# Optimization experiments

Measured on AMD Instinct MI355X. Metric: run time of the kernel, lower is better.

Reference implementation:

```python
import jax, jax.numpy as jnp
import numpy as np
from jax import lax

B, H, W, C = 16, 256, 256, 1
LOC_C = 31            # channels out of localization network
BN_EPS = 1e-3         # Keras BatchNormalization default epsilon
NEG_SLOPE = 0.1       # LeakyReLU slope


def _conv_relu(x, k, b):
    y = lax.conv_general_dilated(x, k, (1, 1), 'SAME',
                                 dimension_numbers=('NHWC', 'HWIO', 'NHWC'))
    return jax.nn.relu(y + b)


def _maxpool2(x):
    return lax.reduce_window(x, -jnp.inf, lax.max, (1, 2, 2, 1), (1, 2, 2, 1), 'VALID')


def _resize_nearest(x, out_h, out_w):
    # tf.image.resize(..., method='nearest') with half-pixel centers
    b, h, w, c = x.shape
    ih = jnp.floor((jnp.arange(out_h) + 0.5) * h / out_h).astype(jnp.int32)
    iw = jnp.floor((jnp.arange(out_w) + 0.5) * w / out_w).astype(jnp.int32)
    return x[:, ih][:, :, iw]


def _generate_grid(theta, height, width):
    # base grid in [-1, 1], x varies along width, y along height
    xs = jnp.arange(width, dtype=jnp.float32) / (width - 1) * 2.0 - 1.0
    ys = jnp.arange(height, dtype=jnp.float32) / (height - 1) * 2.0 - 1.0
    gx, gy = jnp.meshgrid(xs, ys)                      # (H, W)
    grid = jnp.stack([gx, gy], axis=-1).reshape(height * width, 2)  # (HW, 2)
    th = theta.reshape(-1, 2, 3)
    A = th[:, :, :2]                                   # (B, 2, 2)
    t = th[:, :, 2]                                    # (B, 2)
    # NOTE: source does grid @ A (not A @ grid) -- replicate exactly
    tg = jnp.einsum('nc,bcd->bnd', grid, A) + t[:, None, :]
    return tg.reshape(-1, height, width, 2)


def _sampler(img, grid):
    b, h, w, c = img.shape
    x = 0.5 * ((grid[..., 0] + 1.0) * (w - 1))
    y = 0.5 * ((grid[..., 1] + 1.0) * (h - 1))
    x0 = jnp.floor(x); x1 = x0 + 1.0
    y0 = jnp.floor(y); y1 = y0 + 1.0
    x0 = jnp.clip(x0, 0.0, w - 1.0); x1 = jnp.clip(x1, 0.0, w - 1.0)
    y0 = jnp.clip(y0, 0.0, h - 1.0); y1 = jnp.clip(y1, 0.0, h - 1.0)
    wa = (x1 - x) * (y1 - y)
    wb = (x1 - x) * (y - y0)
    wc = (x - x0) * (y1 - y)
    wd = (x - x0) * (y - y0)
    xi0 = x0.astype(jnp.int32); xi1 = x1.astype(jnp.int32)
    yi0 = y0.astype(jnp.int32); yi1 = y1.astype(jnp.int32)
    img_flat = img.reshape(b, h * w, c)

    def gather(yi, xi):
        idx = (yi * w + xi).reshape(b, h * w, 1)       # (B, HW, 1)
        return jnp.take_along_axis(img_flat, idx, axis=1).reshape(b, h, w, c)

    Ia = gather(yi0, xi0)
    Ib = gather(yi1, xi0)
    Ic = gather(yi0, xi1)
    Id = gather(yi1, xi1)
    return (wa[..., None] * Ia + wb[..., None] * Ib
            + wc[..., None] * Ic + wd[..., None] * Id)


def setup_inputs() -> dict:
    key = jax.random.key(0)
    ks = jax.random.split(key, 16)
    s = 0.05
    feat = (H // 8) * (W // 8) * LOC_C  # 31744 flattened localization features
    return {
        'x': jax.random.normal(ks[0], (B, H, W, C), jnp.float32),
        'conv1_k': jax.random.normal(ks[1], (3, 3, C, 8), jnp.float32) * s,
        'conv1_b': jnp.zeros((8,), jnp.float32),
        'conv2_k': jax.random.normal(ks[2], (3, 3, 8, 16), jnp.float32) * s,
        'conv2_b': jnp.zeros((16,), jnp.float32),
        'conv3_k': jax.random.normal(ks[3], (3, 3, 16, LOC_C), jnp.float32) * s,
        'conv3_b': jnp.zeros((LOC_C,), jnp.float32),
        'bn_gamma': 1.0 + 0.1 * jax.random.normal(ks[4], (feat,), jnp.float32),
        'bn_beta': 0.1 * jax.random.normal(ks[5], (feat,), jnp.float32),
        'bn_mean': jnp.zeros((feat,), jnp.float32),
        'bn_var': jnp.ones((feat,), jnp.float32),
        'd1_k': jax.random.normal(ks[6], (feat, 64), jnp.float32) * 0.01,
        'd1_b': jnp.zeros((64,), jnp.float32),
        'd2_k': jax.random.normal(ks[7], (64, 96), jnp.float32) * s,
        'd2_b': jnp.zeros((96,), jnp.float32),
        'd3_k': jax.random.normal(ks[8], (96, 6), jnp.float32) * 0.01,
        'd3_b': jnp.array([1, 0, 0, 0, 1, 0], jnp.float32),
    }


def reference(x, conv1_k, conv1_b, conv2_k, conv2_b, conv3_k, conv3_b,
              bn_gamma, bn_beta, bn_mean, bn_var,
              d1_k, d1_b, d2_k, d2_b, d3_k, d3_b):
    # localization network: (conv-relu, pool) x3 -> (B, H/8, W/8, 31)
    xi = _maxpool2(_conv_relu(x, conv1_k, conv1_b))
    xi = _maxpool2(_conv_relu(xi, conv2_k, conv2_b))
    x_intermediate = _maxpool2(_conv_relu(xi, conv3_k, conv3_b))
    # transformation parameter network (BN in inference mode, dropout = identity)
    f = x_intermediate.reshape(x.shape[0], -1)
    f = (f - bn_mean) * jax.lax.rsqrt(bn_var + BN_EPS) * bn_gamma + bn_beta
    f = jax.nn.relu(f @ d1_k + d1_b)
    f = jax.nn.relu(f @ d2_k + d2_b)
    theta = f @ d3_k + d3_b                            # (B, 6)
    grid = _generate_grid(theta, H, W)                 # (B, H, W, 2)
    loc_up = _resize_nearest(x_intermediate, H, W)     # (B, H, W, 31)
    xc = jnp.concatenate([x, loc_up], axis=-1)         # (B, H, W, 32)
    out = _sampler(xc, grid)
    return jnp.where(out >= 0, out, NEG_SLOPE * out)
```

## Files before the change

kernel.cpp:

```cpp
#include <hip/hip_runtime.h>


#define NEG_SLOPE 0.1f
#define BN_EPS 1e-3f

typedef float vfloat4 __attribute__((ext_vector_type(4)));

__device__ __forceinline__ void fma8(float pv, const float* __restrict__ wk,
                                     float* __restrict__ acc) {
#pragma unroll
    for (int co = 0; co < 8; ++co) acc[co] = fmaf(pv, wk[co], acc[co]);
}

__global__ __launch_bounds__(256, 4) void st_conv1(const float* __restrict__ x,
                                                   const float* __restrict__ w,
                                                   const float* __restrict__ bias,
                                                   float* __restrict__ outA) {
    int idx = blockIdx.x * 256 + threadIdx.x;
    int px = idx & 127, py = (idx >> 7) & 127, b = idx >> 14;
    const float* xb = x + b * 65536;
    int iy0 = 2 * py - 1, ix0 = 2 * px - 1;
    float p[16];
#pragma unroll
    for (int r = 0; r < 4; ++r) {
        int iy = iy0 + r;
        bool oky = (iy >= 0) && (iy < 256);
#pragma unroll
        for (int cc = 0; cc < 4; ++cc) {
            int ix = ix0 + cc;
            bool ok = oky && (ix >= 0) && (ix < 256);
            p[r * 4 + cc] = ok ? xb[iy * 256 + ix] : 0.0f;
        }
    }
    float m[8];
#pragma unroll
    for (int co = 0; co < 8; ++co) m[co] = -1e30f;
#pragma unroll
    for (int oy = 0; oy < 2; ++oy)
#pragma unroll
        for (int ox = 0; ox < 2; ++ox) {
            float acc[8];
#pragma unroll
            for (int co = 0; co < 8; ++co) acc[co] = 0.0f;
#pragma unroll
            for (int ky = 0; ky < 3; ++ky)
#pragma unroll
                for (int kx = 0; kx < 3; ++kx)
                    fma8(p[(oy + ky) * 4 + (ox + kx)], w + (ky * 3 + kx) * 8, acc);
#pragma unroll
            for (int co = 0; co < 8; ++co) m[co] = fmaxf(m[co], acc[co]);
        }
    float4 o0, o1;
    float r0 = m[0] + bias[0], r1 = m[1] + bias[1], r2 = m[2] + bias[2], r3 = m[3] + bias[3];
    float r4 = m[4] + bias[4], r5 = m[5] + bias[5], r6 = m[6] + bias[6], r7 = m[7] + bias[7];
    o0.x = r0 > 0.f ? r0 : 0.f; o0.y = r1 > 0.f ? r1 : 0.f;
    o0.z = r2 > 0.f ? r2 : 0.f; o0.w = r3 > 0.f ? r3 : 0.f;
    o1.x = r4 > 0.f ? r4 : 0.f; o1.y = r5 > 0.f ? r5 : 0.f;
    o1.z = r6 > 0.f ? r6 : 0.f; o1.w = r7 > 0.f ? r7 : 0.f;
    *(float4*)(outA + idx * 8) = o0;
    *(float4*)(outA + idx * 8 + 4) = o1;
}

__global__ __launch_bounds__(256, 2) void st_conv2(const float* __restrict__ A,
                                                   const float* __restrict__ w,
                                                   const float* __restrict__ bias,
                                                   float* __restrict__ outB) {
    int t = threadIdx.x;
    int lane = t & 63;
    int half = __builtin_amdgcn_readfirstlane((t >> 6) & 1);
    int pixel = blockIdx.x * 128 + ((t >> 7) << 6) + lane;
    int px = pixel & 63, py = (pixel >> 6) & 63, b = pixel >> 12;
    const float* Ab = A + b * 128 * 128 * 8;
    int iy0 = 2 * py - 1, ix0 = 2 * px - 1;
    int cobase = half * 8;
    float acc[4][8];
#pragma unroll
    for (int pos = 0; pos < 4; ++pos)
#pragma unroll
        for (int co = 0; co < 8; ++co) acc[pos][co] = 0.0f;

    const float4 z4 = {0.f, 0.f, 0.f, 0.f};
#pragma unroll
    for (int ciq = 0; ciq < 2; ++ciq) {
        float4 p[16];
#pragma unroll
        for (int r = 0; r < 4; ++r) {
            int iy = iy0 + r;
            bool oky = (iy >= 0) && (iy < 128);
#pragma unroll
            for (int cc = 0; cc < 4; ++cc) {
                int ix = ix0 + cc;
                bool ok = oky && (ix >= 0) && (ix < 128);
                p[r * 4 + cc] = ok ? *(const float4*)(Ab + ((iy * 128 + ix) * 8 + ciq * 4))
                                   : z4;
            }
        }
#pragma unroll
        for (int oy = 0; oy < 2; ++oy)
#pragma unroll
            for (int ox = 0; ox < 2; ++ox)
#pragma unroll
                for (int ky = 0; ky < 3; ++ky)
#pragma unroll
                    for (int kx = 0; kx < 3; ++kx) {
                        float4 pv = p[(oy + ky) * 4 + (ox + kx)];
                        const float* wk = w + ((ky * 3 + kx) * 8 + ciq * 4) * 16 + cobase;
                        float* a = acc[oy * 2 + ox];
                        fma8(pv.x, wk, a);
                        fma8(pv.y, wk + 16, a);
                        fma8(pv.z, wk + 32, a);
                        fma8(pv.w, wk + 48, a);
                    }
    }
    float* o = outB + pixel * 16 + cobase;
#pragma unroll
    for (int co = 0; co < 8; ++co) {
        float m = fmaxf(fmaxf(acc[0][co], acc[1][co]),
                        fmaxf(acc[2][co], acc[3][co]));
        m += bias[cobase + co];
        o[co] = m > 0.0f ? m : 0.0f;
    }
}

__global__ __launch_bounds__(256, 4) void st_conv3(const float* __restrict__ Bf,
                                                   const float* __restrict__ w,
                                                   const float* __restrict__ bias,
                                                   float* __restrict__ outC) {
    int t = threadIdx.x;
    int lane = t & 63;
    int q = __builtin_amdgcn_readfirstlane(t >> 6);
    int cobase = q * 8;
    if (cobase > 23) cobase = 23;
    int pixel = blockIdx.x * 64 + lane;
    int ix = pixel & 63, iy = (pixel >> 6) & 63, b = pixel >> 12;
    const float* Bb = Bf + b * 64 * 64 * 16;
    float acc[8];
#pragma unroll
    for (int co = 0; co < 8; ++co) acc[co] = 0.0f;

    const float4 z4 = {0.f, 0.f, 0.f, 0.f};
#pragma unroll
    for (int ciq = 0; ciq < 4; ++ciq) {
        float4 p[9];
#pragma unroll
        for (int ky = 0; ky < 3; ++ky) {
            int y = iy + ky - 1;
            bool oky = (y >= 0) && (y < 64);
#pragma unroll
            for (int kx = 0; kx < 3; ++kx) {
                int xx = ix + kx - 1;
                bool ok = oky && (xx >= 0) && (xx < 64);
                p[ky * 3 + kx] = ok ? *(const float4*)(Bb + ((y * 64 + xx) * 16 + ciq * 4))
                                    : z4;
            }
        }
#pragma unroll
        for (int k = 0; k < 9; ++k) {
            float4 pv = p[k];
            const float* wk = w + (k * 16 + ciq * 4) * 31 + cobase;
            fma8(pv.x, wk, acc);
            fma8(pv.y, wk + 31, acc);
            fma8(pv.z, wk + 62, acc);
            fma8(pv.w, wk + 93, acc);
        }
    }
    float* o = outC + pixel * 32 + cobase;
#pragma unroll
    for (int co = 0; co < 8; ++co) {
        float v = acc[co] + bias[cobase + co];
        o[co] = v > 0.0f ? v : 0.0f;
    }
}

__global__ __launch_bounds__(256) void st_pool3(const float* __restrict__ C3p,
                                                const float* __restrict__ gamma,
                                                const float* __restrict__ beta,
                                                const float* __restrict__ mean,
                                                const float* __restrict__ var,
                                                float* __restrict__ xip,
                                                float* __restrict__ fprime) {
    int idx = blockIdx.x * 256 + threadIdx.x;
    int quad = idx & 7;
    int pp = idx >> 3;
    int b = pp >> 10;
    int cell = pp & 1023;
    int py = cell >> 5, px = cell & 31;
    const float* Cb = C3p + (b * 4096) * 32 + quad * 4;
    float4 v00 = *(const float4*)(Cb + ((2 * py) * 64 + 2 * px) * 32);
    float4 v01 = *(const float4*)(Cb + ((2 * py) * 64 + 2 * px + 1) * 32);
    float4 v10 = *(const float4*)(Cb + ((2 * py + 1) * 64 + 2 * px) * 32);
    float4 v11 = *(const float4*)(Cb + ((2 * py + 1) * 64 + 2 * px + 1) * 32);
    float4 m;
    m.x = fmaxf(fmaxf(v00.x, v01.x), fmaxf(v10.x, v11.x));
    m.y = fmaxf(fmaxf(v00.y, v01.y), fmaxf(v10.y, v11.y));
    m.z = fmaxf(fmaxf(v00.z, v01.z), fmaxf(v10.z, v11.z));
    m.w = fmaxf(fmaxf(v00.w, v01.w), fmaxf(v10.w, v11.w));
    *(float4*)(xip + (b * 1024 + cell) * 32 + quad * 4) = m;
    int c0 = quad * 4;
    float mv[4] = {m.x, m.y, m.z, m.w};
#pragma unroll
    for (int c = 0; c < 4; ++c) {
        int co = c0 + c;
        if (co < 31) {
            int j = cell * 31 + co;
            float sc = gamma[j] * rsqrtf(var[j] + BN_EPS);
            fprime[b * 31744 + j] = (mv[c] - mean[j]) * sc + beta[j];
        }
    }
}

__global__ __launch_bounds__(256) void st_d1(const float* __restrict__ fp,
                                             const float* __restrict__ k1,
                                             float* __restrict__ partial) {
    int t = threadIdx.x, s = blockIdx.x;
    int o = t & 63;
    int sub = t >> 6;
    int subu = __builtin_amdgcn_readfirstlane(sub);
    int j0 = s * 124 + subu * 31;
    float acc[16];
#pragma unroll
    for (int b = 0; b < 16; ++b) acc[b] = 0.0f;
#pragma unroll 4
    for (int jj = 0; jj < 31; ++jj) {
        int j = j0 + jj;
        float kv = k1[j * 64 + o];
        const float* fpj = fp + j;
#pragma unroll
        for (int b = 0; b < 16; ++b)
            acc[b] = fmaf(fpj[b * 31744], kv, acc[b]);
    }
    __shared__ float red[4][16][64];
#pragma unroll
    for (int b = 0; b < 16; ++b) red[sub][b][o] = acc[b];
    __syncthreads();
    if (sub == 0) {
#pragma unroll
        for (int b = 0; b < 16; ++b) {
            float v = red[0][b][o] + red[1][b][o] + red[2][b][o] + red[3][b][o];
            partial[(s * 64 + o) * 16 + b] = v;
        }
    }
}

__global__ __launch_bounds__(256) void st_d1b(const float* __restrict__ partial,
                                              const float* __restrict__ bias,
                                              float* __restrict__ h1) {
    int gid = blockIdx.x * 256 + threadIdx.x;
    int o = gid >> 4, b = gid & 15;
    float s = 0.0f;
#pragma unroll 8
    for (int sl = 0; sl < 256; ++sl) s += partial[(sl * 64 + o) * 16 + b];
    s += bias[o];
    h1[b * 64 + o] = s > 0.0f ? s : 0.0f;
}

__global__ __launch_bounds__(128) void st_theta(const float* __restrict__ h1,
                                                const float* __restrict__ k2,
                                                const float* __restrict__ b2,
                                                const float* __restrict__ k3,
                                                const float* __restrict__ b3,
                                                float* __restrict__ theta) {
    int b = blockIdx.x, t = threadIdx.x;
    __shared__ float h2[96];
    if (t < 96) {
        float s = b2[t];
        for (int i = 0; i < 64; ++i) s = fmaf(h1[b * 64 + i], k2[i * 96 + t], s);
        h2[t] = s > 0.0f ? s : 0.0f;
    }
    __syncthreads();
    if (t < 6) {
        float s = b3[t];
        for (int i = 0; i < 96; ++i) s = fmaf(h2[i], k3[i * 6 + t], s);
        theta[b * 6 + t] = s;
    }
}

__global__ __launch_bounds__(256, 4) void st_sample(const float* __restrict__ x,
                                                    const float* __restrict__ xip,
                                                    const float* __restrict__ theta,
                                                    float* __restrict__ out) {
    __shared__ float smem[256 * 34];
    int t = threadIdx.x;
    int p = blockIdx.x * 256 + t;
    int ow = p & 255, oh = (p >> 8) & 255;
    int b = blockIdx.x >> 8;

    const float* th = theta + b * 6;
    float t0 = th[0], t1 = th[1], t2 = th[2], t3 = th[3], t4 = th[4], t5 = th[5];
    float gx = (float)ow * (2.0f / 255.0f) - 1.0f;
    float gy = (float)oh * (2.0f / 255.0f) - 1.0f;
    float sx = gx * t0 + gy * t3 + t2;
    float sy = gx * t1 + gy * t4 + t5;
    float xf = 0.5f * ((sx + 1.0f) * 255.0f);
    float yf = 0.5f * ((sy + 1.0f) * 255.0f);
    float x0 = floorf(xf), y0 = floorf(yf);
    float x1 = x0 + 1.0f, y1 = y0 + 1.0f;
    x0 = fminf(fmaxf(x0, 0.0f), 255.0f);
    x1 = fminf(fmaxf(x1, 0.0f), 255.0f);
    y0 = fminf(fmaxf(y0, 0.0f), 255.0f);
    y1 = fminf(fmaxf(y1, 0.0f), 255.0f);
    float wa = (x1 - xf) * (y1 - yf);
    float wb = (x1 - xf) * (yf - y0);
    float wc = (xf - x0) * (y1 - yf);
    float wd = (xf - x0) * (yf - y0);
    int xi0 = (int)x0, xi1 = (int)x1, yi0 = (int)y0, yi1 = (int)y1;

    const float* xb = x + b * 65536;
    float Ia = xb[yi0 * 256 + xi0];
    float Ib = xb[yi1 * 256 + xi0];
    float Ic = xb[yi0 * 256 + xi1];
    float Id = xb[yi1 * 256 + xi1];
    float fine = wa * Ia + wb * Ib + wc * Ic + wd * Id;
    fine = fine >= 0.0f ? fine : NEG_SLOPE * fine;

    const float* cellbase = xip + (b << 15);
    const float4* pa = (const float4*)(cellbase + (((yi0 >> 3) << 5) + (xi0 >> 3)) * 32);
    const float4* pb = (const float4*)(cellbase + (((yi1 >> 3) << 5) + (xi0 >> 3)) * 32);
    const float4* pc = (const float4*)(cellbase + (((yi0 >> 3) << 5) + (xi1 >> 3)) * 32);
    const float4* pd = (const float4*)(cellbase + (((yi1 >> 3) << 5) + (xi1 >> 3)) * 32);

    int sbase = t * 34;
    smem[sbase] = fine;
#pragma unroll
    for (int k = 0; k < 8; ++k) {
        float4 va = pa[k], vb = pb[k], vc = pc[k], vd = pd[k];
        float vx = fmaf(wa, va.x, fmaf(wb, vb.x, fmaf(wc, vc.x, wd * vd.x)));
        float vy = fmaf(wa, va.y, fmaf(wb, vb.y, fmaf(wc, vc.y, wd * vd.y)));
        float vz = fmaf(wa, va.z, fmaf(wb, vb.z, fmaf(wc, vc.z, wd * vd.z)));
        float vw = fmaf(wa, va.w, fmaf(wb, vb.w, fmaf(wc, vc.w, wd * vd.w)));
        vx = vx >= 0.0f ? vx : NEG_SLOPE * vx;
        vy = vy >= 0.0f ? vy : NEG_SLOPE * vy;
        vz = vz >= 0.0f ? vz : NEG_SLOPE * vz;
        vw = vw >= 0.0f ? vw : NEG_SLOPE * vw;
        smem[sbase + 1 + 4 * k]     = vx;
        smem[sbase + 2 + 4 * k]     = vy;
        smem[sbase + 3 + 4 * k]     = vz;
        smem[sbase + 4 + 4 * k]     = vw;
    }
    __syncthreads();

    vfloat4* ob = (vfloat4*)(out + blockIdx.x * 8192);
#pragma unroll
    for (int i = 0; i < 8; ++i) {
        int g = i * 256 + t;
        int row = g >> 3, col = 4 * (g & 7);
        float2 lo = *(const float2*)&smem[row * 34 + col];
        float2 hi = *(const float2*)&smem[row * 34 + col + 2];
        vfloat4 v = {lo.x, lo.y, hi.x, hi.y};
        __builtin_nontemporal_store(v, ob + g);
    }
}

extern "C" void kernel_launch(void* const* d_in, const int* in_sizes, int n_in,
                              void* d_out, int out_size, void* d_ws, size_t ws_size,
                              hipStream_t stream) {
    const float* x     = (const float*)d_in[0];
    const float* c1k   = (const float*)d_in[1];
    const float* c1b   = (const float*)d_in[2];
    const float* c2k   = (const float*)d_in[3];
    const float* c2b   = (const float*)d_in[4];
    const float* c3k   = (const float*)d_in[5];
    const float* c3b   = (const float*)d_in[6];
    const float* gamma = (const float*)d_in[7];
    const float* beta  = (const float*)d_in[8];
    const float* mean  = (const float*)d_in[9];
    const float* var   = (const float*)d_in[10];
    const float* d1k   = (const float*)d_in[11];
    const float* d1b   = (const float*)d_in[12];
    const float* d2k   = (const float*)d_in[13];
    const float* d2b   = (const float*)d_in[14];
    const float* d3k   = (const float*)d_in[15];
    const float* d3b   = (const float*)d_in[16];
    float* out = (float*)d_out;
    float* ws  = (float*)d_ws;

    float* A       = ws;
    float* Bf      = ws + 2097152;
    float* C3p     = ws;
    float* xip     = ws + 2097152;
    float* fprime  = ws + 3145728;
    float* partial = ws + 3653632;
    float* h1      = ws + 3915776;
    float* theta   = ws + 3916800;

    st_conv1<<<1024, 256, 0, stream>>>(x, c1k, c1b, A);
    st_conv2<<<512, 256, 0, stream>>>(A, c2k, c2b, Bf);
    st_conv3<<<1024, 256, 0, stream>>>(Bf, c3k, c3b, C3p);
    st_pool3<<<512, 256, 0, stream>>>(C3p, gamma, beta, mean, var, xip, fprime);
    st_d1<<<256, 256, 0, stream>>>(fprime, d1k, partial);
    st_d1b<<<4, 256, 0, stream>>>(partial, d1b, h1);
    st_theta<<<16, 128, 0, stream>>>(h1, d2k, d2b, d3k, d3b, theta);
    st_sample<<<4096, 256, 0, stream>>>(x, xip, theta, out);
}
```

Measured before the change: 279.4 us.

## Fuse conv3 with maxpool and BN, split sampler channels across threads

Conv3 now computes the four conv outputs of each 2x2 pool window per thread. In the same kernel it applies max-pool, bias, ReLU and the BatchNorm affine, then writes the pooled map and the normalized features directly. This removes the full-resolution conv3 intermediate and the separate pool kernel. The dense-1 reduction is rebalanced to half as many slices, each twice as long. The sampler drops its shared-memory transpose: four threads per output pixel each handle 8 channels and store them directly. The trade-off is that the fused conv3 launches only 256 blocks with more registers per thread, which may leave the GPU underoccupied.

```diff
diff --git a/kernel.cpp b/kernel.cpp
--- a/kernel.cpp
+++ b/kernel.cpp
@@ -122,90 +122,77 @@
     }
 }
 
-__global__ __launch_bounds__(256, 4) void st_conv3(const float* __restrict__ Bf,
-                                                   const float* __restrict__ w,
-                                                   const float* __restrict__ bias,
-                                                   float* __restrict__ outC) {
+__global__ __launch_bounds__(256, 2) void st_conv3p(const float* __restrict__ Bf,
+                                                    const float* __restrict__ w,
+                                                    const float* __restrict__ bias,
+                                                    const float* __restrict__ gamma,
+                                                    const float* __restrict__ beta,
+                                                    const float* __restrict__ mean,
+                                                    const float* __restrict__ var,
+                                                    float* __restrict__ xip,
+                                                    float* __restrict__ fprime) {
     int t = threadIdx.x;
     int lane = t & 63;
     int q = __builtin_amdgcn_readfirstlane(t >> 6);
     int cobase = q * 8;
     if (cobase > 23) cobase = 23;
     int pixel = blockIdx.x * 64 + lane;
-    int ix = pixel & 63, iy = (pixel >> 6) & 63, b = pixel >> 12;
+    int b = pixel >> 10;
+    int cell = pixel & 1023;
+    int ppy = cell >> 5, ppx = cell & 31;
     const float* Bb = Bf + b * 64 * 64 * 16;
-    float acc[8];
-#pragma unroll
-    for (int co = 0; co < 8; ++co) acc[co] = 0.0f;
+    int iy0 = 2 * ppy - 1, ix0 = 2 * ppx - 1;
+    float acc[4][8];
+#pragma unroll
+    for (int pos = 0; pos < 4; ++pos)
+#pragma unroll
+        for (int co = 0; co < 8; ++co) acc[pos][co] = 0.0f;
 
     const float4 z4 = {0.f, 0.f, 0.f, 0.f};
 #pragma unroll
     for (int ciq = 0; ciq < 4; ++ciq) {
-        float4 p[9];
-#pragma unroll
-        for (int ky = 0; ky < 3; ++ky) {
-            int y = iy + ky - 1;
+        float4 p[16];
+#pragma unroll
+        for (int r = 0; r < 4; ++r) {
+            int y = iy0 + r;
             bool oky = (y >= 0) && (y < 64);
 #pragma unroll
-            for (int kx = 0; kx < 3; ++kx) {
-                int xx = ix + kx - 1;
+            for (int cc = 0; cc < 4; ++cc) {
+                int xx = ix0 + cc;
                 bool ok = oky && (xx >= 0) && (xx < 64);
-                p[ky * 3 + kx] = ok ? *(const float4*)(Bb + ((y * 64 + xx) * 16 + ciq * 4))
-                                    : z4;
+                p[r * 4 + cc] = ok ? *(const float4*)(Bb + ((y * 64 + xx) * 16 + ciq * 4))
+                                   : z4;
             }
         }
 #pragma unroll
-        for (int k = 0; k < 9; ++k) {
-            float4 pv = p[k];
-            const float* wk = w + (k * 16 + ciq * 4) * 31 + cobase;
-            fma8(pv.x, wk, acc);
-            fma8(pv.y, wk + 31, acc);
-            fma8(pv.z, wk + 62, acc);
-            fma8(pv.w, wk + 93, acc);
-        }
-    }
-    float* o = outC + pixel * 32 + cobase;
+        for (int oy = 0; oy < 2; ++oy)
+#pragma unroll
+            for (int ox = 0; ox < 2; ++ox)
+#pragma unroll
+                for (int ky = 0; ky < 3; ++ky)
+#pragma unroll
+                    for (int kx = 0; kx < 3; ++kx) {
+                        float4 pv = p[(oy + ky) * 4 + (ox + kx)];
+                        const float* wk = w + ((ky * 3 + kx) * 16 + ciq * 4) * 31 + cobase;
+                        float* a = acc[oy * 2 + ox];
+                        fma8(pv.x, wk, a);
+                        fma8(pv.y, wk + 31, a);
+                        fma8(pv.z, wk + 62, a);
+                        fma8(pv.w, wk + 93, a);
+                    }
+    }
+    float* xcell = xip + (b << 15) + cell * 32 + 1 + cobase;
+    float* fpb = fprime + b * 31744;
 #pragma unroll
     for (int co = 0; co < 8; ++co) {
-        float v = acc[co] + bias[cobase + co];
-        o[co] = v > 0.0f ? v : 0.0f;
-    }
-}
-
-__global__ __launch_bounds__(256) void st_pool3(const float* __restrict__ C3p,
-                                                const float* __restrict__ gamma,
-                                                const float* __restrict__ beta,
-                                                const float* __restrict__ mean,
-                                                const float* __restrict__ var,
-                                                float* __restrict__ xip,
-                                                float* __restrict__ fprime) {
-    int idx = blockIdx.x * 256 + threadIdx.x;
-    int quad = idx & 7;
-    int pp = idx >> 3;
-    int b = pp >> 10;
-    int cell = pp & 1023;
-    int py = cell >> 5, px = cell & 31;
-    const float* Cb = C3p + (b * 4096) * 32 + quad * 4;
-    float4 v00 = *(const float4*)(Cb + ((2 * py) * 64 + 2 * px) * 32);
-    float4 v01 = *(const float4*)(Cb + ((2 * py) * 64 + 2 * px + 1) * 32);
-    float4 v10 = *(const float4*)(Cb + ((2 * py + 1) * 64 + 2 * px) * 32);
-    float4 v11 = *(const float4*)(Cb + ((2 * py + 1) * 64 + 2 * px + 1) * 32);
-    float4 m;
-    m.x = fmaxf(fmaxf(v00.x, v01.x), fmaxf(v10.x, v11.x));
-    m.y = fmaxf(fmaxf(v00.y, v01.y), fmaxf(v10.y, v11.y));
-    m.z = fmaxf(fmaxf(v00.z, v01.z), fmaxf(v10.z, v11.z));
-    m.w = fmaxf(fmaxf(v00.w, v01.w), fmaxf(v10.w, v11.w));
-    *(float4*)(xip + (b * 1024 + cell) * 32 + quad * 4) = m;
-    int c0 = quad * 4;
-    float mv[4] = {m.x, m.y, m.z, m.w};
-#pragma unroll
-    for (int c = 0; c < 4; ++c) {
-        int co = c0 + c;
-        if (co < 31) {
-            int j = cell * 31 + co;
-            float sc = gamma[j] * rsqrtf(var[j] + BN_EPS);
-            fprime[b * 31744 + j] = (mv[c] - mean[j]) * sc + beta[j];
-        }
+        float m = fmaxf(fmaxf(acc[0][co], acc[1][co]),
+                        fmaxf(acc[2][co], acc[3][co]));
+        m += bias[cobase + co];
+        float v = m > 0.0f ? m : 0.0f;
+        xcell[co] = v;
+        int j = cell * 31 + cobase + co;
+        float sc = gamma[j] * rsqrtf(var[j] + BN_EPS);
+        fpb[j] = (v - mean[j]) * sc + beta[j];
     }
 }
 
@@ -216,12 +203,12 @@
     int o = t & 63;
     int sub = t >> 6;
     int subu = __builtin_amdgcn_readfirstlane(sub);
-    int j0 = s * 124 + subu * 31;
+    int j0 = s * 248 + subu * 62;
     float acc[16];
 #pragma unroll
     for (int b = 0; b < 16; ++b) acc[b] = 0.0f;
-#pragma unroll 4
-    for (int jj = 0; jj < 31; ++jj) {
+#pragma unroll 2
+    for (int jj = 0; jj < 62; ++jj) {
         int j = j0 + jj;
         float kv = k1[j * 64 + o];
         const float* fpj = fp + j;
@@ -249,7 +236,7 @@
     int o = gid >> 4, b = gid & 15;
     float s = 0.0f;
 #pragma unroll 8
-    for (int sl = 0; sl < 256; ++sl) s += partial[(sl * 64 + o) * 16 + b];
+    for (int sl = 0; sl < 128; ++sl) s += partial[(sl * 64 + o) * 16 + b];
     s += bias[o];
     h1[b * 64 + o] = s > 0.0f ? s : 0.0f;
 }
@@ -275,15 +262,15 @@
     }
 }
 
-__global__ __launch_bounds__(256, 4) void st_sample(const float* __restrict__ x,
-                                                    const float* __restrict__ xip,
-                                                    const float* __restrict__ theta,
-                                                    float* __restrict__ out) {
-    __shared__ float smem[256 * 34];
-    int t = threadIdx.x;
-    int p = blockIdx.x * 256 + t;
-    int ow = p & 255, oh = (p >> 8) & 255;
-    int b = blockIdx.x >> 8;
+__global__ __launch_bounds__(256) void st_sample(const float* __restrict__ x,
+                                                 const float* __restrict__ xip,
+                                                 const float* __restrict__ theta,
+                                                 float* __restrict__ out) {
+    int gid = blockIdx.x * 256 + threadIdx.x;
+    int q = gid & 3;
+    int pix = gid >> 2;
+    int ow = pix & 255, oh = (pix >> 8) & 255;
+    int b = __builtin_amdgcn_readfirstlane(blockIdx.x >> 10);
 
     const float* th = theta + b * 6;
     float t0 = th[0], t1 = th[1], t2 = th[2], t3 = th[3], t4 = th[4], t5 = th[5];
@@ -305,50 +292,41 @@
     float wd = (xf - x0) * (yf - y0);
     int xi0 = (int)x0, xi1 = (int)x1, yi0 = (int)y0, yi1 = (int)y1;
 
-    const float* xb = x + b * 65536;
-    float Ia = xb[yi0 * 256 + xi0];
-    float Ib = xb[yi1 * 256 + xi0];
-    float Ic = xb[yi0 * 256 + xi1];
-    float Id = xb[yi1 * 256 + xi1];
-    float fine = wa * Ia + wb * Ib + wc * Ic + wd * Id;
-    fine = fine >= 0.0f ? fine : NEG_SLOPE * fine;
-
     const float* cellbase = xip + (b << 15);
-    const float4* pa = (const float4*)(cellbase + (((yi0 >> 3) << 5) + (xi0 >> 3)) * 32);
-    const float4* pb = (const float4*)(cellbase + (((yi1 >> 3) << 5) + (xi0 >> 3)) * 32);
-    const float4* pc = (const float4*)(cellbase + (((yi0 >> 3) << 5) + (xi1 >> 3)) * 32);
-    const float4* pd = (const float4*)(cellbase + (((yi1 >> 3) << 5) + (xi1 >> 3)) * 32);
-
-    int sbase = t * 34;
-    smem[sbase] = fine;
-#pragma unroll
-    for (int k = 0; k < 8; ++k) {
-        float4 va = pa[k], vb = pb[k], vc = pc[k], vd = pd[k];
-        float vx = fmaf(wa, va.x, fmaf(wb, vb.x, fmaf(wc, vc.x, wd * vd.x)));
-        float vy = fmaf(wa, va.y, fmaf(wb, vb.y, fmaf(wc, vc.y, wd * vd.y)));
-        float vz = fmaf(wa, va.z, fmaf(wb, vb.z, fmaf(wc, vc.z, wd * vd.z)));
-        float vw = fmaf(wa, va.w, fmaf(wb, vb.w, fmaf(wc, vc.w, wd * vd.w)));
-        vx = vx >= 0.0f ? vx : NEG_SLOPE * vx;
-        vy = vy >= 0.0f ? vy : NEG_SLOPE * vy;
-        vz = vz >= 0.0f ? vz : NEG_SLOPE * vz;
-        vw = vw >= 0.0f ? vw : NEG_SLOPE * vw;
-        smem[sbase + 1 + 4 * k]     = vx;
-        smem[sbase + 2 + 4 * k]     = vy;
-        smem[sbase + 3 + 4 * k]     = vz;
-        smem[sbase + 4 + 4 * k]     = vw;
-    }
-    __syncthreads();
-
-    vfloat4* ob = (vfloat4*)(out + blockIdx.x * 8192);
-#pragma unroll
-    for (int i = 0; i < 8; ++i) {
-        int g = i * 256 + t;
-        int row = g >> 3, col = 4 * (g & 7);
-        float2 lo = *(const float2*)&smem[row * 34 + col];
-        float2 hi = *(const float2*)&smem[row * 34 + col + 2];
-        vfloat4 v = {lo.x, lo.y, hi.x, hi.y};
-        __builtin_nontemporal_store(v, ob + g);
-    }
+    int off = q * 8;
+    const float* pa = cellbase + ((((yi0 >> 3) << 5) + (xi0 >> 3)) << 5) + off;
+    const float* pb = cellbase + ((((yi1 >> 3) << 5) + (xi0 >> 3)) << 5) + off;
+    const float* pc = cellbase + ((((yi0 >> 3) << 5) + (xi1 >> 3)) << 5) + off;
+    const float* pd = cellbase + ((((yi1 >> 3) << 5) + (xi1 >> 3)) << 5) + off;
+
+    float r[8];
+#pragma unroll
+    for (int k = 0; k < 2; ++k) {
+        float4 va = *(const float4*)(pa + 4 * k);
+        float4 vb = *(const float4*)(pb + 4 * k);
+        float4 vc = *(const float4*)(pc + 4 * k);
+        float4 vd = *(const float4*)(pd + 4 * k);
+        r[4 * k]     = fmaf(wa, va.x, fmaf(wb, vb.x, fmaf(wc, vc.x, wd * vd.x)));
+        r[4 * k + 1] = fmaf(wa, va.y, fmaf(wb, vb.y, fmaf(wc, vc.y, wd * vd.y)));
+        r[4 * k + 2] = fmaf(wa, va.z, fmaf(wb, vb.z, fmaf(wc, vc.z, wd * vd.z)));
+        r[4 * k + 3] = fmaf(wa, va.w, fmaf(wb, vb.w, fmaf(wc, vc.w, wd * vd.w)));
+    }
+    if (q == 0) {
+        const float* xb = x + b * 65536;
+        float Ia = xb[yi0 * 256 + xi0];
+        float Ib = xb[yi1 * 256 + xi0];
+        float Ic = xb[yi0 * 256 + xi1];
+        float Id = xb[yi1 * 256 + xi1];
+        r[0] = fmaf(wa, Ia, fmaf(wb, Ib, fmaf(wc, Ic, wd * Id)));
+    }
+#pragma unroll
+    for (int i = 0; i < 8; ++i) r[i] = r[i] >= 0.0f ? r[i] : NEG_SLOPE * r[i];
+
+    float* ob = out + pix * 32 + off;
+    vfloat4 v0 = {r[0], r[1], r[2], r[3]};
+    vfloat4 v1 = {r[4], r[5], r[6], r[7]};
+    __builtin_nontemporal_store(v0, (vfloat4*)ob);
+    __builtin_nontemporal_store(v1, (vfloat4*)(ob + 4));
 }
 
 extern "C" void kernel_launch(void* const* d_in, const int* in_sizes, int n_in,
@@ -376,19 +354,18 @@
 
     float* A       = ws;
     float* Bf      = ws + 2097152;
-    float* C3p     = ws;
-    float* xip     = ws + 2097152;
-    float* fprime  = ws + 3145728;
-    float* partial = ws + 3653632;
-    float* h1      = ws + 3915776;
-    float* theta   = ws + 3916800;
+    float* xip     = ws;
+    float* fprime  = ws + 524288;
+    float* partial = ws + 3145728;
+    float* h1      = ws + 3276800;
+    float* theta   = ws + 3277824;
 
     st_conv1<<<1024, 256, 0, stream>>>(x, c1k, c1b, A);
     st_conv2<<<512, 256, 0, stream>>>(A, c2k, c2b, Bf);
-    st_conv3<<<1024, 256, 0, stream>>>(Bf, c3k, c3b, C3p);
-    st_pool3<<<512, 256, 0, stream>>>(C3p, gamma, beta, mean, var, xip, fprime);
-    st_d1<<<256, 256, 0, stream>>>(fprime, d1k, partial);
+    st_conv3p<<<256, 256, 0, stream>>>(Bf, c3k, c3b, gamma, beta, mean, var,
+                                       xip, fprime);
+    st_d1<<<128, 256, 0, stream>>>(fprime, d1k, partial);
     st_d1b<<<4, 256, 0, stream>>>(partial, d1b, h1);
     st_theta<<<16, 128, 0, stream>>>(h1, d2k, d2b, d3k, d3b, theta);
-    st_sample<<<4096, 256, 0, stream>>>(x, xip, theta, out);
-}
+    st_sample<<<16384, 256, 0, stream>>>(x, xip, theta, out);
+}
```

Result: slower. 415.9 us (+48.8%).
